# Optimization experiments

Measured on AMD Instinct MI355X. Metric: run time of the kernel, lower is better.

## Reference

```python
import jax, jax.numpy as jnp
import numpy as np
from jax import lax

B, C, OUT, K, H, W = 8, 64, 32, 3, 64, 64


def _conv2d(x, w, b, stride=1, pad=0, groups=1):
    o = lax.conv_general_dilated(x, w, (stride, stride), [(pad, pad), (pad, pad)],
                                 dimension_numbers=('NCHW', 'OIHW', 'NCHW'),
                                 feature_group_count=groups)
    return o + b[None, :, None, None]


def _bn(x, g, b, m, v, eps=1e-5):
    # eval-mode BatchNorm2d with running stats
    s = g / jnp.sqrt(v + eps)
    return x * s[None, :, None, None] + (b - m * s)[None, :, None, None]


def _eca(x, w):
    # global avg pool -> 1D conv over channel axis -> sigmoid gate [b,c,1,1]
    y = x.mean((-2, -1))[:, None, :]  # [b,1,c]
    y = lax.conv_general_dilated(y, w, (1,), [(1, 1)],
                                 dimension_numbers=('NCW', 'OIW', 'NCW'))
    return jax.nn.sigmoid(y[:, 0, :])[:, :, None, None]


def _avgpool3(x):
    # AvgPool2d(k=3, stride=1, pad=1), count_include_pad=True (torch default)
    s = lax.reduce_window(x, 0.0, lax.add, (1, 1, 3, 3), (1, 1, 1, 1),
                          [(0, 0), (0, 0), (1, 1), (1, 1)])
    return s / 9.0


def _forward(x, sc_w, sc_b, ac_w, ac_b, oc_w, oc_b, oc_bn_g, oc_bn_b, oc_bn_m, oc_bn_v,
             ex_w, ey_w, ez_w, ff_w, ff_b, g1_w, g1_b, g2_w, g2_b,
             fu_w, fu_b, fu_bn_g, fu_bn_b, fu_bn_m, fu_bn_v):
    b, c, h, w = x.shape
    k = K
    # --- ReceptiveFieldAttentionConv ---
    frf = jax.nn.silu(_conv2d(x, sc_w, sc_b, pad=k // 2, groups=c))
    frf = frf.reshape(b, c, k * k, h, w)
    arf = _conv2d(_avgpool3(x), ac_w, ac_b, groups=c).reshape(b, c, k * k, h, w)
    arf = jax.nn.softmax(arf, axis=2)  # softmax over k*k RF positions
    wt = (frf * arf).reshape(b, c, k, k, h, w)
    wt = wt.transpose(0, 1, 4, 2, 5, 3).reshape(b, c, h * k, w * k)  # pixel-shuffle-like
    x_rfa = jax.nn.silu(_bn(_conv2d(wt, oc_w, oc_b, stride=k, groups=4),
                            oc_bn_g, oc_bn_b, oc_bn_m, oc_bn_v))
    # --- FrequencyGroupedChannelAttention ---
    energy = jnp.abs(jnp.fft.fft2(x)).mean((-2, -1))  # [b,c]
    ranks = jnp.argsort(jnp.argsort(-energy, axis=1), axis=1)
    mask = (ranks < c // 2).astype(x.dtype)[:, :, None, None]  # top-half-energy channels
    a_x = _eca(x, ex_w)
    a_y = _eca(x * mask, ey_w)
    a_z = _eca(x * (1.0 - mask), ez_w)
    a_f = _conv2d(jnp.concatenate([a_y, a_z], 1), ff_w, ff_b, groups=4)
    g_in = jnp.concatenate([a_f, a_x], 1)
    g = jax.nn.sigmoid(_conv2d(jax.nn.silu(_conv2d(g_in, g1_w, g1_b)), g2_w, g2_b))
    x_fgca = x * (g * a_f + (1.0 - g) * a_x)
    # --- fuse ---
    fused = jnp.concatenate([x_rfa, x_fgca], 1)
    return jax.nn.silu(_bn(_conv2d(fused, fu_w, fu_b),
                           fu_bn_g, fu_bn_b, fu_bn_m, fu_bn_v))


def setup_inputs() -> dict:
    key = jax.random.key(0)
    ks = jax.random.split(key, 32)
    rn = lambda k, shp, s=0.1: jax.random.normal(k, shp, jnp.float32) * s
    gh = max(8, C // 4)  # gate hidden = 16
    return {
        'x': jax.random.normal(ks[0], (B, C, H, W), jnp.float32),
        'sc_w': rn(ks[1], (C * K * K, 1, K, K)), 'sc_b': rn(ks[2], (C * K * K,)),
        'ac_w': rn(ks[3], (C * K * K, 1, 1, 1)), 'ac_b': rn(ks[4], (C * K * K,)),
        'oc_w': rn(ks[5], (C, C // 4, K, K)), 'oc_b': rn(ks[6], (C,)),
        'oc_bn_g': 1.0 + rn(ks[7], (C,)), 'oc_bn_b': rn(ks[8], (C,)),
        'oc_bn_m': rn(ks[9], (C,)), 'oc_bn_v': 0.9 + 0.2 * jax.random.uniform(ks[10], (C,), jnp.float32),
        'ex_w': rn(ks[11], (1, 1, 3), 0.3), 'ey_w': rn(ks[12], (1, 1, 3), 0.3),
        'ez_w': rn(ks[13], (1, 1, 3), 0.3),
        'ff_w': rn(ks[14], (C, 2 * C // 4, 1, 1)), 'ff_b': rn(ks[15], (C,)),
        'g1_w': rn(ks[16], (gh, 2 * C, 1, 1)), 'g1_b': rn(ks[17], (gh,)),
        'g2_w': rn(ks[18], (C, gh, 1, 1)), 'g2_b': rn(ks[19], (C,)),
        'fu_w': rn(ks[20], (OUT, 2 * C, 1, 1)), 'fu_b': rn(ks[21], (OUT,)),
        'fu_bn_g': 1.0 + rn(ks[22], (OUT,)), 'fu_bn_b': rn(ks[23], (OUT,)),
        'fu_bn_m': rn(ks[24], (OUT,)), 'fu_bn_v': 0.9 + 0.2 * jax.random.uniform(ks[25], (OUT,), jnp.float32),
    }


def reference(x, sc_w, sc_b, ac_w, ac_b, oc_w, oc_b, oc_bn_g, oc_bn_b, oc_bn_m, oc_bn_v,
              ex_w, ey_w, ez_w, ff_w, ff_b, g1_w, g1_b, g2_w, g2_b,
              fu_w, fu_b, fu_bn_g, fu_bn_b, fu_bn_m, fu_bn_v):
    return _forward(x, sc_w, sc_b, ac_w, ac_b, oc_w, oc_b, oc_bn_g, oc_bn_b, oc_bn_m, oc_bn_v,
                    ex_w, ey_w, ez_w, ff_w, ff_b, g1_w, g1_b, g2_w, g2_b,
                    fu_w, fu_b, fu_bn_g, fu_bn_b, fu_bn_m, fu_bn_v)
```

## Files before the change

kernel.cpp:

```cpp
#include <hip/hip_runtime.h>
#include <math.h>

#define EPS 1e-5f

__device__ __forceinline__ float wave_sum(float v) {
  v += __shfl_down(v, 32);
  v += __shfl_down(v, 16);
  v += __shfl_down(v, 8);
  v += __shfl_down(v, 4);
  v += __shfl_down(v, 2);
  v += __shfl_down(v, 1);
  return v;
}

__device__ __forceinline__ float silu_f(float v) { return v / (1.f + __expf(-v)); }
__device__ __forceinline__ float sigm_f(float v) { return 1.f / (1.f + __expf(-v)); }

__device__ __forceinline__ int bitrev6(int v) {
  return ((v & 1) << 5) | ((v & 2) << 3) | ((v & 4) << 1) |
         ((v & 8) >> 1) | ((v & 16) >> 3) | ((v & 32) >> 5);
}

#define FFT6(zr, zi)                                           \
  do {                                                         \
    _Pragma("unroll") for (int s = 0; s < 6; ++s) {            \
      const int half = 32 >> s;                                \
      const bool up = (lane & half) != 0;                      \
      float pr = __shfl_xor(zr, half);                         \
      float pi = __shfl_xor(zi, half);                         \
      float tr = up ? pr - zr : zr + pr;                       \
      float ti = up ? pi - zi : zi + pi;                       \
      const float c = twc[s], sn = tws[s];                     \
      zr = tr * c - ti * sn;                                   \
      zi = tr * sn + ti * c;                                   \
    }                                                          \
  } while (0)

__global__ __launch_bounds__(256) void k_dft(const float* __restrict__ x,
                                             float* __restrict__ energy,
                                             float* __restrict__ meanx) {
  __shared__ float re1[33 * 65];
  __shared__ float im1[33 * 65];
  __shared__ float redA[4], redB[4];
  const int bc = blockIdx.x;
  const int tid = threadIdx.x;
  const int lane = tid & 63;
  const int wv = tid >> 6;
  const float* xp = x + (size_t)bc * 4096;

  float twc[6], tws[6];
#pragma unroll
  for (int s = 0; s < 6; ++s) {
    int half = 32 >> s;
    if (lane & half) {
      float ang = -6.283185307179586f * (float)((lane & (half - 1)) << s) / 64.f;
      float sv, cv;
      __sincosf(ang, &sv, &cv);
      twc[s] = cv;
      tws[s] = sv;
    } else {
      twc[s] = 1.f;
      tws[s] = 0.f;
    }
  }

  const int f = bitrev6(lane);
  const int fm = (64 - f) & 63;
  const int plane = bitrev6(fm);

  float lsum = 0.f;
#pragma unroll 1
  for (int rp = 0; rp < 4; ++rp) {
    const int h0 = wv * 16 + rp * 4;
    float x0 = xp[h0 * 64 + lane];
    float x1 = xp[(h0 + 1) * 64 + lane];
    float x2 = xp[(h0 + 2) * 64 + lane];
    float x3 = xp[(h0 + 3) * 64 + lane];
    lsum += x0 + x1 + x2 + x3;
    float zr = x0, zi = x1, yr = x2, yi = x3;
#pragma unroll
    for (int s = 0; s < 6; ++s) {
      const int half = 32 >> s;
      const bool up = (lane & half) != 0;
      float pzr = __shfl_xor(zr, half);
      float pzi = __shfl_xor(zi, half);
      float pyr = __shfl_xor(yr, half);
      float pyi = __shfl_xor(yi, half);
      float tzr = up ? pzr - zr : zr + pzr;
      float tzi = up ? pzi - zi : zi + pzi;
      float tyr = up ? pyr - yr : yr + pyr;
      float tyi = up ? pyi - yi : yi + pyi;
      const float c = twc[s], sn = tws[s];
      zr = tzr * c - tzi * sn;
      zi = tzr * sn + tzi * c;
      yr = tyr * c - tyi * sn;
      yi = tyr * sn + tyi * c;
    }
    float mzr = __shfl(zr, plane), mzi = __shfl(zi, plane);
    float myr = __shfl(yr, plane), myi = __shfl(yi, plane);
    if (f <= 32) {
      float ar = 0.5f * (zr + mzr), ai = 0.5f * (zi - mzi);
      float br = 0.5f * (zi + mzi), bi = 0.5f * (mzr - zr);
      float cr = 0.5f * (yr + myr), ci = 0.5f * (yi - myi);
      float dr = 0.5f * (yi + myi), di = 0.5f * (myr - yr);
      re1[f * 65 + h0] = ar;     im1[f * 65 + h0] = ai;
      re1[f * 65 + h0 + 1] = br; im1[f * 65 + h0 + 1] = bi;
      re1[f * 65 + h0 + 2] = cr; im1[f * 65 + h0 + 2] = ci;
      re1[f * 65 + h0 + 3] = dr; im1[f * 65 + h0 + 3] = di;
    }
  }
  __syncthreads();

  float msum = 0.f;
#pragma unroll 1
  for (int i = 0; i < 4; ++i) {
    const int kv1 = wv + 8 * i;
    const int kv2 = kv1 + 4;
    const float w1 = (kv1 == 0) ? 1.f : 2.f;
    float ar = re1[kv1 * 65 + lane];
    float ai = im1[kv1 * 65 + lane];
    float br = re1[kv2 * 65 + lane];
    float bi = im1[kv2 * 65 + lane];
#pragma unroll
    for (int s = 0; s < 6; ++s) {
      const int half = 32 >> s;
      const bool up = (lane & half) != 0;
      float par = __shfl_xor(ar, half);
      float pai = __shfl_xor(ai, half);
      float pbr = __shfl_xor(br, half);
      float pbi = __shfl_xor(bi, half);
      float tar = up ? par - ar : ar + par;
      float tai = up ? pai - ai : ai + pai;
      float tbr = up ? pbr - br : br + pbr;
      float tbi = up ? pbi - bi : bi + pbi;
      const float c = twc[s], sn = tws[s];
      ar = tar * c - tai * sn;
      ai = tar * sn + tai * c;
      br = tbr * c - tbi * sn;
      bi = tbr * sn + tbi * c;
    }
    msum += w1 * sqrtf(ar * ar + ai * ai) + 2.f * sqrtf(br * br + bi * bi);
  }
  if (wv == 0) {
    float ar = re1[32 * 65 + lane];
    float ai = im1[32 * 65 + lane];
    FFT6(ar, ai);
    msum += sqrtf(ar * ar + ai * ai);
  }

  msum = wave_sum(msum);
  lsum = wave_sum(lsum);
  if (lane == 0) { redA[wv] = msum; redB[wv] = lsum; }
  __syncthreads();
  if (tid == 0) {
    float e = redA[0] + redA[1] + redA[2] + redA[3];
    float m = redB[0] + redB[1] + redB[2] + redB[3];
    energy[bc] = e * (1.f / 4096.f);
    meanx[bc] = m * (1.f / 4096.f);
  }
}

__global__ __launch_bounds__(64) void k_attn(
    const float* __restrict__ energy, const float* __restrict__ meanx,
    const float* __restrict__ ex_w, const float* __restrict__ ey_w,
    const float* __restrict__ ez_w, const float* __restrict__ ff_w,
    const float* __restrict__ ff_b, const float* __restrict__ g1_w,
    const float* __restrict__ g1_b, const float* __restrict__ g2_w,
    const float* __restrict__ g2_b, float* __restrict__ s2) {
  __shared__ float e[64], mx[64], my[64], mz[64];
  __shared__ float ax[64], ay[64], az[64], af[64], h1[16];
  const int b = blockIdx.x;
  const int c = threadIdx.x;
  e[c] = energy[b * 64 + c];
  mx[c] = meanx[b * 64 + c];
  __syncthreads();
  int rank = 0;
  float ec = e[c];
  for (int i = 0; i < 64; ++i) {
    float ei = e[i];
    rank += (ei > ec) || (ei == ec && i < c);
  }
  float mask = (rank < 32) ? 1.f : 0.f;
  my[c] = mx[c] * mask;
  mz[c] = mx[c] * (1.f - mask);
  __syncthreads();
  {
    float l, r, m;
    l = (c > 0) ? mx[c - 1] : 0.f; m = mx[c]; r = (c < 63) ? mx[c + 1] : 0.f;
    ax[c] = sigm_f(ex_w[0] * l + ex_w[1] * m + ex_w[2] * r);
    l = (c > 0) ? my[c - 1] : 0.f; m = my[c]; r = (c < 63) ? my[c + 1] : 0.f;
    ay[c] = sigm_f(ey_w[0] * l + ey_w[1] * m + ey_w[2] * r);
    l = (c > 0) ? mz[c - 1] : 0.f; m = mz[c]; r = (c < 63) ? mz[c + 1] : 0.f;
    az[c] = sigm_f(ez_w[0] * l + ez_w[1] * m + ez_w[2] * r);
  }
  __syncthreads();
  {
    int g = c >> 4;
    float acc = ff_b[c];
#pragma unroll
    for (int i = 0; i < 32; ++i) {
      int ch = g * 32 + i;
      float v = (ch < 64) ? ay[ch] : az[ch - 64];
      acc = fmaf(v, ff_w[c * 32 + i], acc);
    }
    af[c] = acc;
  }
  __syncthreads();
  if (c < 16) {
    float a = g1_b[c];
#pragma unroll
    for (int i = 0; i < 64; ++i) a = fmaf(af[i], g1_w[c * 128 + i], a);
#pragma unroll
    for (int i = 0; i < 64; ++i) a = fmaf(ax[i], g1_w[c * 128 + 64 + i], a);
    h1[c] = silu_f(a);
  }
  __syncthreads();
  float gv = g2_b[c];
#pragma unroll
  for (int o = 0; o < 16; ++o) gv = fmaf(h1[o], g2_w[c * 16 + o], gv);
  gv = sigm_f(gv);
  s2[b * 64 + c] = gv * af[c] + (1.f - gv) * ax[c];
}

__global__ __launch_bounds__(256) void k_rfa(
    const float* __restrict__ x,
    const float* __restrict__ sc_w, const float* __restrict__ sc_b,
    const float* __restrict__ ac_w, const float* __restrict__ ac_b,
    const float* __restrict__ oc_w, const float* __restrict__ oc_b,
    const float* __restrict__ bn_g, const float* __restrict__ bn_b,
    const float* __restrict__ bn_m, const float* __restrict__ bn_v,
    float* __restrict__ xrfa) {
  __shared__ __align__(16) float scwp[16 * 9 * 12];
  __shared__ __align__(16) float mp[16 * 24];
  __shared__ __align__(16) float ocwp[16 * 16 * 12];
  __shared__ float red[128 * 33];
  const int blk = blockIdx.x;
  const int band = blk & 15;
  const int g = (blk >> 4) & 3;
  const int b = blk >> 6;
  const int tid = threadIdx.x;
  const int lane = tid & 63;
  const int wv = tid >> 6;
  const int wp = wv & 1;
  const int half = wv >> 1;

  for (int i = tid; i < 1296; i += 256) {
    int icg = i / 81, rem = i - icg * 81;
    int j = rem / 9, t = rem - j * 9;
    scwp[icg * 108 + j * 12 + t] = sc_w[(g * 144 + icg * 9 + j) * 9 + t];
  }
  if (tid < 144) {
    int icg = tid / 9, j = tid - icg * 9;
    scwp[icg * 108 + j * 12 + 9] = sc_b[g * 144 + tid];
    mp[icg * 24 + j] = ac_w[g * 144 + tid];
    mp[icg * 24 + 12 + j] = ac_b[g * 144 + tid];
  }
  for (int i = tid; i < 2304; i += 256) {
    int oco = i / 144, rem = i - oco * 144;
    int icg = rem / 9, j = rem - icg * 9;
    ocwp[icg * 192 + oco * 12 + j] = oc_w[((g * 16 + oco) * 16 + icg) * 9 + j];
  }
  __syncthreads();

  const int r0 = band * 4 + wp * 2;
  const int w = lane;
  const bool vW = w > 0, vE = w < 63;
  float acc0[16], acc1[16];
#pragma unroll
  for (int i = 0; i < 16; ++i) { acc0[i] = 0.f; acc1[i] = 0.f; }

  const float* xg = x + ((size_t)(b * 64 + g * 16)) * 4096 + w;
  const int icg0 = half * 8;

#pragma unroll 1
  for (int ii = 0; ii < 8; ++ii) {
    const int icg = icg0 + ii;
    const float* xc = xg + icg * 4096;
    float n[12];
#pragma unroll
    for (int t = 0; t < 4; ++t) {
      int h = r0 - 1 + t;
      bool vh = (h >= 0) && (h < 64);
      const float* row = xc + h * 64;
      n[t * 3 + 0] = (vh && vW) ? row[-1] : 0.f;
      n[t * 3 + 1] = vh ? row[0] : 0.f;
      n[t * 3 + 2] = (vh && vE) ? row[1] : 0.f;
    }
    float rs0 = n[0] + n[1] + n[2];
    float rs1 = n[3] + n[4] + n[5];
    float rs2 = n[6] + n[7] + n[8];
    float rs3 = n[9] + n[10] + n[11];
    float ap0 = (rs0 + rs1 + rs2) * (1.f / 9.f);
    float ap1 = (rs1 + rs2 + rs3) * (1.f / 9.f);

    float aw[12], ab[12];
    *(float4*)&aw[0] = *(const float4*)&mp[icg * 24];
    *(float4*)&aw[4] = *(const float4*)&mp[icg * 24 + 4];
    *(float4*)&aw[8] = *(const float4*)&mp[icg * 24 + 8];
    *(float4*)&ab[0] = *(const float4*)&mp[icg * 24 + 12];
    *(float4*)&ab[4] = *(const float4*)&mp[icg * 24 + 16];
    *(float4*)&ab[8] = *(const float4*)&mp[icg * 24 + 20];

    float f0[9], f1[9], a0[9], a1[9];
    float amax0 = -1e30f, amax1 = -1e30f;
#pragma unroll
    for (int j = 0; j < 9; ++j) {
      float wt[12];
      *(float4*)&wt[0] = *(const float4*)&scwp[icg * 108 + j * 12];
      *(float4*)&wt[4] = *(const float4*)&scwp[icg * 108 + j * 12 + 4];
      *(float4*)&wt[8] = *(const float4*)&scwp[icg * 108 + j * 12 + 8];
      float p0 = wt[9], p1 = wt[9];
#pragma unroll
      for (int t = 0; t < 9; ++t) {
        p0 = fmaf(n[t], wt[t], p0);
        p1 = fmaf(n[t + 3], wt[t], p1);
      }
      f0[j] = silu_f(p0);
      f1[j] = silu_f(p1);
      float v0 = fmaf(ap0, aw[j], ab[j]);
      float v1 = fmaf(ap1, aw[j], ab[j]);
      a0[j] = v0; a1[j] = v1;
      amax0 = fmaxf(amax0, v0);
      amax1 = fmaxf(amax1, v1);
    }
    float es0 = 0.f, es1 = 0.f;
    float p0[9], p1[9];
#pragma unroll
    for (int j = 0; j < 9; ++j) {
      float e0 = __expf(a0[j] - amax0);
      float e1 = __expf(a1[j] - amax1);
      es0 += e0; es1 += e1;
      p0[j] = f0[j] * e0;
      p1[j] = f1[j] * e1;
    }
    float i0 = __fdividef(1.f, es0);
    float i1 = __fdividef(1.f, es1);
#pragma unroll
    for (int j = 0; j < 9; ++j) { p0[j] *= i0; p1[j] *= i1; }

#pragma unroll
    for (int oco = 0; oco < 16; ++oco) {
      float ov[12];
      *(float4*)&ov[0] = *(const float4*)&ocwp[icg * 192 + oco * 12];
      *(float4*)&ov[4] = *(const float4*)&ocwp[icg * 192 + oco * 12 + 4];
      *(float4*)&ov[8] = *(const float4*)&ocwp[icg * 192 + oco * 12 + 8];
      float s0 = 0.f, s1 = 0.f;
#pragma unroll
      for (int j = 0; j < 9; ++j) {
        s0 = fmaf(p0[j], ov[j], s0);
        s1 = fmaf(p1[j], ov[j], s1);
      }
      acc0[oco] += s0;
      acc1[oco] += s1;
    }
  }

  const int rid = wp * 64 + lane;
  if (half == 1) {
#pragma unroll
    for (int k = 0; k < 16; ++k) {
      red[rid * 33 + k] = acc0[k];
      red[rid * 33 + 16 + k] = acc1[k];
    }
  }
  __syncthreads();
  if (half == 0) {
#pragma unroll
    for (int k = 0; k < 16; ++k) {
      acc0[k] += red[rid * 33 + k];
      acc1[k] += red[rid * 33 + 16 + k];
    }
    float* op = xrfa + ((size_t)(b * 64 + g * 16)) * 4096 + r0 * 64 + w;
#pragma unroll
    for (int oco = 0; oco < 16; ++oco) {
      int oc = g * 16 + oco;
      float s = bn_g[oc] * rsqrtf(bn_v[oc] + EPS);
      float bb = bn_b[oc] - bn_m[oc] * s;
      float ob = oc_b[oc];
      float v0 = fmaf(acc0[oco] + ob, s, bb);
      float v1 = fmaf(acc1[oco] + ob, s, bb);
      op[oco * 4096] = silu_f(v0);
      op[oco * 4096 + 64] = silu_f(v1);
    }
  }
}

__global__ __launch_bounds__(256) void k_fuse(
    const float* __restrict__ x, const float* __restrict__ xrfa,
    const float* __restrict__ s2, const float* __restrict__ fu_w,
    const float* __restrict__ fu_b, const float* __restrict__ bn_g,
    const float* __restrict__ bn_b, const float* __restrict__ bn_m,
    const float* __restrict__ bn_v, float* __restrict__ out) {
  __shared__ __align__(16) float fw[4096];
  __shared__ float s2l[64];
  const int blk = blockIdx.x;
  const int tid = threadIdx.x;
  const int sloc = tid & 63;
  const int ocq = tid >> 6;
  const int b = blk >> 6;
  const int sp = (blk & 63) * 64 + sloc;

  for (int i = tid; i < 1024; i += 256)
    ((float4*)fw)[i] = ((const float4*)fu_w)[i];
  if (tid < 64) s2l[tid] = s2[b * 64 + tid];

  const float* xr = xrfa + (size_t)b * 64 * 4096 + sp;
  const float* xp = x + (size_t)b * 64 * 4096 + sp;
  float va[64], vb[64];
#pragma unroll
  for (int i = 0; i < 64; ++i) va[i] = xr[i * 4096];
#pragma unroll
  for (int i = 0; i < 64; ++i) vb[i] = xp[i * 4096];
  __syncthreads();
#pragma unroll
  for (int i = 0; i < 64; ++i) vb[i] *= s2l[i];

  float* op = out + (size_t)b * 32 * 4096 + sp;
#pragma unroll 1
  for (int o = 0; o < 8; ++o) {
    const int oc = ocq * 8 + o;
    const float* wr = &fw[oc * 128];
    float a = 0.f;
#pragma unroll
    for (int q = 0; q < 16; ++q) {
      float4 w4 = *(const float4*)&wr[q * 4];
      a = fmaf(va[q * 4 + 0], w4.x, a);
      a = fmaf(va[q * 4 + 1], w4.y, a);
      a = fmaf(va[q * 4 + 2], w4.z, a);
      a = fmaf(va[q * 4 + 3], w4.w, a);
    }
#pragma unroll
    for (int q = 0; q < 16; ++q) {
      float4 w4 = *(const float4*)&wr[64 + q * 4];
      a = fmaf(vb[q * 4 + 0], w4.x, a);
      a = fmaf(vb[q * 4 + 1], w4.y, a);
      a = fmaf(vb[q * 4 + 2], w4.z, a);
      a = fmaf(vb[q * 4 + 3], w4.w, a);
    }
    float s = bn_g[oc] * rsqrtf(bn_v[oc] + EPS);
    float v = a + fu_b[oc];
    v = fmaf(v, s, bn_b[oc] - bn_m[oc] * s);
    op[oc * 4096] = silu_f(v);
  }
}

extern "C" void kernel_launch(void* const* d_in, const int* in_sizes, int n_in,
                              void* d_out, int out_size, void* d_ws, size_t ws_size,
                              hipStream_t stream) {
  const float* x       = (const float*)d_in[0];
  const float* sc_w    = (const float*)d_in[1];
  const float* sc_b    = (const float*)d_in[2];
  const float* ac_w    = (const float*)d_in[3];
  const float* ac_b    = (const float*)d_in[4];
  const float* oc_w    = (const float*)d_in[5];
  const float* oc_b    = (const float*)d_in[6];
  const float* oc_bn_g = (const float*)d_in[7];
  const float* oc_bn_b = (const float*)d_in[8];
  const float* oc_bn_m = (const float*)d_in[9];
  const float* oc_bn_v = (const float*)d_in[10];
  const float* ex_w    = (const float*)d_in[11];
  const float* ey_w    = (const float*)d_in[12];
  const float* ez_w    = (const float*)d_in[13];
  const float* ff_w    = (const float*)d_in[14];
  const float* ff_b    = (const float*)d_in[15];
  const float* g1_w    = (const float*)d_in[16];
  const float* g1_b    = (const float*)d_in[17];
  const float* g2_w    = (const float*)d_in[18];
  const float* g2_b    = (const float*)d_in[19];
  const float* fu_w    = (const float*)d_in[20];
  const float* fu_b    = (const float*)d_in[21];
  const float* fu_bn_g = (const float*)d_in[22];
  const float* fu_bn_b = (const float*)d_in[23];
  const float* fu_bn_m = (const float*)d_in[24];
  const float* fu_bn_v = (const float*)d_in[25];

  float* ws     = (float*)d_ws;
  float* energy = ws;
  float* meanx  = ws + 512;
  float* s2     = ws + 1024;
  float* xrfa   = ws + 2048;

  k_dft<<<512, 256, 0, stream>>>(x, energy, meanx);
  k_attn<<<8, 64, 0, stream>>>(energy, meanx, ex_w, ey_w, ez_w,
                               ff_w, ff_b, g1_w, g1_b, g2_w, g2_b, s2);
  k_rfa<<<512, 256, 0, stream>>>(x, sc_w, sc_b, ac_w, ac_b, oc_w, oc_b,
                                 oc_bn_g, oc_bn_b, oc_bn_m, oc_bn_v, xrfa);
  k_fuse<<<512, 256, 0, stream>>>(x, xrfa, s2, fu_w, fu_b,
                                  fu_bn_g, fu_bn_b, fu_bn_m, fu_bn_v,
                                  (float*)d_out);
}
```

Baseline: 174.1 us.

## Fuse attention into FFT kernel via last-block counter; widen RFA per-thread rows

The channel-attention kernel is folded into the FFT/energy kernel. Each block atomically bumps a per-batch counter, and the last block for a batch computes the gating vector, which removes one launch at the cost of an added memset. Separately, the RFA kernel now has each wave compute four output rows over four input channels instead of two rows over eight. A two-stage shared-memory reduction combines the partial results, and launch_bounds asks for two blocks per CU. This gives more reuse of the loaded neighbourhood across rows, but raises register pressure (64 accumulators) and uses much more LDS for the reduction.

After: 193.2 us. 11.0% more time.

```diff
diff --git a/kernel.cpp b/kernel.cpp
--- a/kernel.cpp
+++ b/kernel.cpp
@@ -36,12 +36,18 @@
     }                                                          \
   } while (0)
 
-__global__ __launch_bounds__(256) void k_dft(const float* __restrict__ x,
-                                             float* __restrict__ energy,
-                                             float* __restrict__ meanx) {
+__global__ __launch_bounds__(256) void k_dft(
+    const float* __restrict__ x, float* __restrict__ energy,
+    float* __restrict__ meanx, int* __restrict__ cnt,
+    const float* __restrict__ ex_w, const float* __restrict__ ey_w,
+    const float* __restrict__ ez_w, const float* __restrict__ ff_w,
+    const float* __restrict__ ff_b, const float* __restrict__ g1_w,
+    const float* __restrict__ g1_b, const float* __restrict__ g2_w,
+    const float* __restrict__ g2_b, float* __restrict__ s2) {
   __shared__ float re1[33 * 65];
   __shared__ float im1[33 * 65];
   __shared__ float redA[4], redB[4];
+  __shared__ int isLast;
   const int bc = blockIdx.x;
   const int tid = threadIdx.x;
   const int lane = tid & 63;
@@ -158,33 +164,45 @@
     energy[bc] = e * (1.f / 4096.f);
     meanx[bc] = m * (1.f / 4096.f);
   }
-}
-
-__global__ __launch_bounds__(64) void k_attn(
-    const float* __restrict__ energy, const float* __restrict__ meanx,
-    const float* __restrict__ ex_w, const float* __restrict__ ey_w,
-    const float* __restrict__ ez_w, const float* __restrict__ ff_w,
-    const float* __restrict__ ff_b, const float* __restrict__ g1_w,
-    const float* __restrict__ g1_b, const float* __restrict__ g2_w,
-    const float* __restrict__ g2_b, float* __restrict__ s2) {
-  __shared__ float e[64], mx[64], my[64], mz[64];
-  __shared__ float ax[64], ay[64], az[64], af[64], h1[16];
-  const int b = blockIdx.x;
-  const int c = threadIdx.x;
-  e[c] = energy[b * 64 + c];
-  mx[c] = meanx[b * 64 + c];
-  __syncthreads();
-  int rank = 0;
-  float ec = e[c];
-  for (int i = 0; i < 64; ++i) {
-    float ei = e[i];
-    rank += (ei > ec) || (ei == ec && i < c);
-  }
-  float mask = (rank < 32) ? 1.f : 0.f;
-  my[c] = mx[c] * mask;
-  mz[c] = mx[c] * (1.f - mask);
-  __syncthreads();
-  {
+
+  if (tid == 0) {
+    __threadfence();
+    int old = atomicAdd(&cnt[bc >> 6], 1);
+    isLast = (old == 63) ? 1 : 0;
+  }
+  __syncthreads();
+  if (!isLast) return;
+  __threadfence();
+
+  const int b = bc >> 6;
+  float* e  = &re1[0];
+  float* mx = &re1[64];
+  float* my = &re1[128];
+  float* mz = &re1[192];
+  float* ax = &re1[256];
+  float* ay = &re1[320];
+  float* az = &re1[384];
+  float* af = &re1[448];
+  float* h1 = &re1[512];
+  const int c = tid;
+  if (c < 64) {
+    e[c] = energy[b * 64 + c];
+    mx[c] = meanx[b * 64 + c];
+  }
+  __syncthreads();
+  if (c < 64) {
+    int rank = 0;
+    float ec = e[c];
+    for (int i = 0; i < 64; ++i) {
+      float ei = e[i];
+      rank += (ei > ec) || (ei == ec && i < c);
+    }
+    float mask = (rank < 32) ? 1.f : 0.f;
+    my[c] = mx[c] * mask;
+    mz[c] = mx[c] * (1.f - mask);
+  }
+  __syncthreads();
+  if (c < 64) {
     float l, r, m;
     l = (c > 0) ? mx[c - 1] : 0.f; m = mx[c]; r = (c < 63) ? mx[c + 1] : 0.f;
     ax[c] = sigm_f(ex_w[0] * l + ex_w[1] * m + ex_w[2] * r);
@@ -194,12 +212,12 @@
     az[c] = sigm_f(ez_w[0] * l + ez_w[1] * m + ez_w[2] * r);
   }
   __syncthreads();
-  {
-    int g = c >> 4;
+  if (c < 64) {
+    int gg = c >> 4;
     float acc = ff_b[c];
 #pragma unroll
     for (int i = 0; i < 32; ++i) {
-      int ch = g * 32 + i;
+      int ch = gg * 32 + i;
       float v = (ch < 64) ? ay[ch] : az[ch - 64];
       acc = fmaf(v, ff_w[c * 32 + i], acc);
     }
@@ -215,14 +233,16 @@
     h1[c] = silu_f(a);
   }
   __syncthreads();
-  float gv = g2_b[c];
-#pragma unroll
-  for (int o = 0; o < 16; ++o) gv = fmaf(h1[o], g2_w[c * 16 + o], gv);
-  gv = sigm_f(gv);
-  s2[b * 64 + c] = gv * af[c] + (1.f - gv) * ax[c];
+  if (c < 64) {
+    float gv = g2_b[c];
+#pragma unroll
+    for (int o = 0; o < 16; ++o) gv = fmaf(h1[o], g2_w[c * 16 + o], gv);
+    gv = sigm_f(gv);
+    s2[b * 64 + c] = gv * af[c] + (1.f - gv) * ax[c];
+  }
 }
 
-__global__ __launch_bounds__(256) void k_rfa(
+__global__ __launch_bounds__(256, 2) void k_rfa(
     const float* __restrict__ x,
     const float* __restrict__ sc_w, const float* __restrict__ sc_b,
     const float* __restrict__ ac_w, const float* __restrict__ ac_b,
@@ -233,7 +253,7 @@
   __shared__ __align__(16) float scwp[16 * 9 * 12];
   __shared__ __align__(16) float mp[16 * 24];
   __shared__ __align__(16) float ocwp[16 * 16 * 12];
-  __shared__ float red[128 * 33];
+  __shared__ float red[2 * 64 * 65];
   const int blk = blockIdx.x;
   const int band = blk & 15;
   const int g = (blk >> 4) & 3;
@@ -241,8 +261,6 @@
   const int tid = threadIdx.x;
   const int lane = tid & 63;
   const int wv = tid >> 6;
-  const int wp = wv & 1;
-  const int half = wv >> 1;
 
   for (int i = tid; i < 1296; i += 256) {
     int icg = i / 81, rem = i - icg * 81;
@@ -262,23 +280,23 @@
   }
   __syncthreads();
 
-  const int r0 = band * 4 + wp * 2;
+  const int r0 = band * 4;
   const int w = lane;
   const bool vW = w > 0, vE = w < 63;
-  float acc0[16], acc1[16];
-#pragma unroll
-  for (int i = 0; i < 16; ++i) { acc0[i] = 0.f; acc1[i] = 0.f; }
+  float acc[64];
+#pragma unroll
+  for (int i = 0; i < 64; ++i) acc[i] = 0.f;
 
   const float* xg = x + ((size_t)(b * 64 + g * 16)) * 4096 + w;
-  const int icg0 = half * 8;
+  const int icg0 = wv * 4;
 
 #pragma unroll 1
-  for (int ii = 0; ii < 8; ++ii) {
+  for (int ii = 0; ii < 4; ++ii) {
     const int icg = icg0 + ii;
     const float* xc = xg + icg * 4096;
-    float n[12];
-#pragma unroll
-    for (int t = 0; t < 4; ++t) {
+    float n[18];
+#pragma unroll
+    for (int t = 0; t < 6; ++t) {
       int h = r0 - 1 + t;
       bool vh = (h >= 0) && (h < 64);
       const float* row = xc + h * 64;
@@ -286,12 +304,12 @@
       n[t * 3 + 1] = vh ? row[0] : 0.f;
       n[t * 3 + 2] = (vh && vE) ? row[1] : 0.f;
     }
-    float rs0 = n[0] + n[1] + n[2];
-    float rs1 = n[3] + n[4] + n[5];
-    float rs2 = n[6] + n[7] + n[8];
-    float rs3 = n[9] + n[10] + n[11];
-    float ap0 = (rs0 + rs1 + rs2) * (1.f / 9.f);
-    float ap1 = (rs1 + rs2 + rs3) * (1.f / 9.f);
+    float rs[6];
+#pragma unroll
+    for (int t = 0; t < 6; ++t) rs[t] = n[t * 3] + n[t * 3 + 1] + n[t * 3 + 2];
+    float ap[4];
+#pragma unroll
+    for (int p = 0; p < 4; ++p) ap[p] = (rs[p] + rs[p + 1] + rs[p + 2]) * (1.f / 9.f);
 
     float aw[12], ab[12];
     *(float4*)&aw[0] = *(const float4*)&mp[icg * 24];
@@ -301,42 +319,41 @@
     *(float4*)&ab[4] = *(const float4*)&mp[icg * 24 + 16];
     *(float4*)&ab[8] = *(const float4*)&mp[icg * 24 + 20];
 
-    float f0[9], f1[9], a0[9], a1[9];
-    float amax0 = -1e30f, amax1 = -1e30f;
+    float f[4][9];
+    float amax[4] = {-1e30f, -1e30f, -1e30f, -1e30f};
 #pragma unroll
     for (int j = 0; j < 9; ++j) {
       float wt[12];
       *(float4*)&wt[0] = *(const float4*)&scwp[icg * 108 + j * 12];
       *(float4*)&wt[4] = *(const float4*)&scwp[icg * 108 + j * 12 + 4];
       *(float4*)&wt[8] = *(const float4*)&scwp[icg * 108 + j * 12 + 8];
-      float p0 = wt[9], p1 = wt[9];
-#pragma unroll
-      for (int t = 0; t < 9; ++t) {
-        p0 = fmaf(n[t], wt[t], p0);
-        p1 = fmaf(n[t + 3], wt[t], p1);
+#pragma unroll
+      for (int p = 0; p < 4; ++p) {
+        float pre = wt[9];
+#pragma unroll
+        for (int t = 0; t < 9; ++t) pre = fmaf(n[p * 3 + t], wt[t], pre);
+        f[p][j] = silu_f(pre);
+        float av = fmaf(ap[p], aw[j], ab[j]);
+        amax[p] = fmaxf(amax[p], av);
       }
-      f0[j] = silu_f(p0);
-      f1[j] = silu_f(p1);
-      float v0 = fmaf(ap0, aw[j], ab[j]);
-      float v1 = fmaf(ap1, aw[j], ab[j]);
-      a0[j] = v0; a1[j] = v1;
-      amax0 = fmaxf(amax0, v0);
-      amax1 = fmaxf(amax1, v1);
-    }
-    float es0 = 0.f, es1 = 0.f;
-    float p0[9], p1[9];
+    }
+    float es[4] = {0.f, 0.f, 0.f, 0.f};
 #pragma unroll
     for (int j = 0; j < 9; ++j) {
-      float e0 = __expf(a0[j] - amax0);
-      float e1 = __expf(a1[j] - amax1);
-      es0 += e0; es1 += e1;
-      p0[j] = f0[j] * e0;
-      p1[j] = f1[j] * e1;
-    }
-    float i0 = __fdividef(1.f, es0);
-    float i1 = __fdividef(1.f, es1);
-#pragma unroll
-    for (int j = 0; j < 9; ++j) { p0[j] *= i0; p1[j] *= i1; }
+#pragma unroll
+      for (int p = 0; p < 4; ++p) {
+        float av = fmaf(ap[p], aw[j], ab[j]);
+        float ev = __expf(av - amax[p]);
+        es[p] += ev;
+        f[p][j] *= ev;
+      }
+    }
+#pragma unroll
+    for (int p = 0; p < 4; ++p) {
+      float inv = __fdividef(1.f, es[p]);
+#pragma unroll
+      for (int j = 0; j < 9; ++j) f[p][j] *= inv;
+    }
 
 #pragma unroll
     for (int oco = 0; oco < 16; ++oco) {
@@ -344,41 +361,60 @@
       *(float4*)&ov[0] = *(const float4*)&ocwp[icg * 192 + oco * 12];
       *(float4*)&ov[4] = *(const float4*)&ocwp[icg * 192 + oco * 12 + 4];
       *(float4*)&ov[8] = *(const float4*)&ocwp[icg * 192 + oco * 12 + 8];
-      float s0 = 0.f, s1 = 0.f;
-#pragma unroll
-      for (int j = 0; j < 9; ++j) {
-        s0 = fmaf(p0[j], ov[j], s0);
-        s1 = fmaf(p1[j], ov[j], s1);
+#pragma unroll
+      for (int p = 0; p < 4; ++p) {
+        float s = 0.f;
+#pragma unroll
+        for (int j = 0; j < 9; ++j) s = fmaf(f[p][j], ov[j], s);
+        acc[p * 16 + oco] += s;
       }
-      acc0[oco] += s0;
-      acc1[oco] += s1;
-    }
-  }
-
-  const int rid = wp * 64 + lane;
-  if (half == 1) {
-#pragma unroll
-    for (int k = 0; k < 16; ++k) {
-      red[rid * 33 + k] = acc0[k];
-      red[rid * 33 + 16 + k] = acc1[k];
-    }
-  }
-  __syncthreads();
-  if (half == 0) {
-#pragma unroll
-    for (int k = 0; k < 16; ++k) {
-      acc0[k] += red[rid * 33 + k];
-      acc1[k] += red[rid * 33 + 16 + k];
-    }
-    float* op = xrfa + ((size_t)(b * 64 + g * 16)) * 4096 + r0 * 64 + w;
+    }
+  }
+
+  if (wv >= 2) {
+    float* rp = &red[(wv - 2) * 64 * 65 + lane * 65];
+#pragma unroll
+    for (int k = 0; k < 64; ++k) rp[k] = acc[k];
+  }
+  __syncthreads();
+  if (wv < 2) {
+    const float* rp = &red[wv * 64 * 65 + lane * 65];
+#pragma unroll
+    for (int k = 0; k < 64; ++k) acc[k] += rp[k];
+  }
+  __syncthreads();
+  if (wv == 1) {
+    float* rp = &red[lane * 65];
+#pragma unroll
+    for (int k = 0; k < 32; ++k) rp[k] = acc[k];
+  } else if (wv == 0) {
+    float* rp = &red[64 * 65 + lane * 65];
+#pragma unroll
+    for (int k = 0; k < 32; ++k) rp[k] = acc[32 + k];
+  }
+  __syncthreads();
+
+  if (wv < 2) {
+    const int pbase = wv * 2;
+    float av[32];
+    if (wv == 0) {
+      const float* rp = &red[lane * 65];
+#pragma unroll
+      for (int k = 0; k < 32; ++k) av[k] = acc[k] + rp[k];
+    } else {
+      const float* rp = &red[64 * 65 + lane * 65];
+#pragma unroll
+      for (int k = 0; k < 32; ++k) av[k] = acc[32 + k] + rp[k];
+    }
+    float* op = xrfa + ((size_t)(b * 64 + g * 16)) * 4096 + (r0 + pbase) * 64 + w;
 #pragma unroll
     for (int oco = 0; oco < 16; ++oco) {
       int oc = g * 16 + oco;
       float s = bn_g[oc] * rsqrtf(bn_v[oc] + EPS);
       float bb = bn_b[oc] - bn_m[oc] * s;
       float ob = oc_b[oc];
-      float v0 = fmaf(acc0[oco] + ob, s, bb);
-      float v1 = fmaf(acc1[oco] + ob, s, bb);
+      float v0 = fmaf(av[oco] + ob, s, bb);
+      float v1 = fmaf(av[16 + oco] + ob, s, bb);
       op[oco * 4096] = silu_f(v0);
       op[oco * 4096 + 64] = silu_f(v1);
     }
@@ -478,11 +514,13 @@
   float* energy = ws;
   float* meanx  = ws + 512;
   float* s2     = ws + 1024;
+  int*   cnt    = (int*)(ws + 1536);
   float* xrfa   = ws + 2048;
 
-  k_dft<<<512, 256, 0, stream>>>(x, energy, meanx);
-  k_attn<<<8, 64, 0, stream>>>(energy, meanx, ex_w, ey_w, ez_w,
-                               ff_w, ff_b, g1_w, g1_b, g2_w, g2_b, s2);
+  hipMemsetAsync(cnt, 0, 8 * sizeof(int), stream);
+  k_dft<<<512, 256, 0, stream>>>(x, energy, meanx, cnt,
+                                 ex_w, ey_w, ez_w, ff_w, ff_b,
+                                 g1_w, g1_b, g2_w, g2_b, s2);
   k_rfa<<<512, 256, 0, stream>>>(x, sc_w, sc_b, ac_w, ac_b, oc_w, oc_b,
                                  oc_bn_g, oc_bn_b, oc_bn_m, oc_bn_v, xrfa);
   k_fuse<<<512, 256, 0, stream>>>(x, xrfa, s2, fu_w, fu_b,
```
